# Kernel optimization log

Hardware: AMD Instinct MI355X
Metric: run time of the kernel (lower is better)

The kernel has to match this reference:

```python
import jax, jax.numpy as jnp
import numpy as np

E = 524288
B = 16
NODE_IN = 128
EDGE_IN = 64
GLOBAL_IN = 64
HIDDEN = 256
EDGE_OUT = 64
CAT_IN = EDGE_IN + 2 * NODE_IN + GLOBAL_IN  # 384


def setup_inputs() -> dict:
    key = jax.random.key(0)
    ks = jax.random.split(key, 9)
    src = jax.random.normal(ks[0], (E, NODE_IN), dtype=jnp.float32)
    dest = jax.random.normal(ks[1], (E, NODE_IN), dtype=jnp.float32)
    edge_attr = jax.random.normal(ks[2], (E, EDGE_IN), dtype=jnp.float32)
    u = jax.random.normal(ks[3], (B, GLOBAL_IN), dtype=jnp.float32)
    batch = jnp.sort(jax.random.randint(ks[4], (E,), 0, B, dtype=jnp.int64))
    # MLP params (torch Linear default init scale ~1/sqrt(fan_in))
    W1 = jax.random.normal(ks[5], (CAT_IN, HIDDEN), dtype=jnp.float32) / np.sqrt(CAT_IN)
    b1 = jax.random.normal(ks[6], (HIDDEN,), dtype=jnp.float32) / np.sqrt(CAT_IN)
    W2 = jax.random.normal(ks[7], (HIDDEN, EDGE_OUT), dtype=jnp.float32) / np.sqrt(HIDDEN)
    b2 = jax.random.normal(ks[8], (EDGE_OUT,), dtype=jnp.float32) / np.sqrt(HIDDEN)
    return {"src": src, "dest": dest, "edge_attr": edge_attr, "u": u,
            "batch": batch, "W1": W1, "b1": b1, "W2": W2, "b2": b2}


def reference(src, dest, edge_attr, u, batch, W1, b1, W2, b2):
    # gather global features per edge, concat, 2-layer MLP with ReLU
    x = jnp.concatenate([src, dest, edge_attr, u[batch]], axis=1)  # [E, 384]
    h = jax.nn.relu(x @ W1 + b1)                                   # [E, hidden]
    return h @ W2 + b2                                             # [E, edge_out]
```

## Files before the change

kernel.cpp:

```cpp
#include <hip/hip_runtime.h>

typedef __bf16 bf16_t;
typedef bf16_t bf16x8 __attribute__((ext_vector_type(8)));
typedef float f32x4 __attribute__((ext_vector_type(4)));
typedef unsigned short u16;
typedef u16 u16x8 __attribute__((ext_vector_type(8)));
typedef unsigned int u32;
typedef u32 u32x4 __attribute__((ext_vector_type(4)));

#define E_TOT 524288
#define MT 64
#define NBLK (E_TOT / MT)

__device__ __forceinline__ u16 f2bf(float f) {
  u32 u = __builtin_bit_cast(u32, f);
  u += 0x7FFFu + ((u >> 16) & 1u);
  return (u16)(u >> 16);
}

__device__ __forceinline__ u16x8 pack8(f32x4 a, f32x4 b) {
  u16x8 p;
  p[0] = f2bf(a[0]); p[1] = f2bf(a[1]); p[2] = f2bf(a[2]); p[3] = f2bf(a[3]);
  p[4] = f2bf(b[0]); p[5] = f2bf(b[1]); p[6] = f2bf(b[2]); p[7] = f2bf(b[3]);
  return p;
}

__global__ void prep_w1t(const float* __restrict__ W1, u16* __restrict__ W1T) {
  int t = blockIdx.x * 256 + threadIdx.x;
  if (t < 256 * 384) {
    int n = t / 384, k = t % 384;
    W1T[t] = f2bf(W1[k * 256 + n]);
  }
}
__global__ void prep_w2t(const float* __restrict__ W2, u16* __restrict__ W2T) {
  int t = blockIdx.x * 256 + threadIdx.x;
  if (t < 64 * 256) {
    int n = t / 256, k = t % 256;
    W2T[t] = f2bf(W2[k * 64 + n]);
  }
}

__global__ void __launch_bounds__(256) edge_fused(
    const float* __restrict__ src, const float* __restrict__ dst,
    const float* __restrict__ ea, const float* __restrict__ u,
    const int* __restrict__ batch, const u16* __restrict__ W1T,
    const float* __restrict__ b1, const u16* __restrict__ W2T,
    const float* __restrict__ b2, float* __restrict__ out)
{
  __shared__ __align__(16) u16 smem[32768];
  u16* As  = smem;
  u16* Ws  = smem + 4608;
  u16* Hs  = smem;
  u16* W2s = smem + 16384;

  const int t    = threadIdx.x;
  const int wid  = t >> 6;
  const int lane = t & 63;
  const int lr   = lane & 15;
  const int lg   = lane >> 4;
  const int e0   = blockIdx.x * MT;

  f32x4 acc[4][4];
  #pragma unroll
  for (int i = 0; i < 4; ++i)
    #pragma unroll
    for (int j = 0; j < 4; ++j)
      acc[i][j] = (f32x4){0.f, 0.f, 0.f, 0.f};

  const int r  = t >> 2;
  const int cg = (t & 3) << 4;

  #pragma unroll
  for (int kb = 0; kb < 6; ++kb) {
    __syncthreads();
    const float* rowp;
    if (kb < 2)       rowp = src + (e0 + r) * 128 + kb * 64;
    else if (kb < 4)  rowp = dst + (e0 + r) * 128 + (kb - 2) * 64;
    else if (kb == 4) rowp = ea + (e0 + r) * 64;
    else              rowp = u + batch[e0 + r] * 64;
    f32x4 v0 = *(const f32x4*)(rowp + cg + 0);
    f32x4 v1 = *(const f32x4*)(rowp + cg + 4);
    f32x4 v2 = *(const f32x4*)(rowp + cg + 8);
    f32x4 v3 = *(const f32x4*)(rowp + cg + 12);
    *(u16x8*)&As[r * 72 + cg + 0] = pack8(v0, v1);
    *(u16x8*)&As[r * 72 + cg + 8] = pack8(v2, v3);

    #pragma unroll
    for (int it = 0; it < 8; ++it) {
      int idx = t + it * 256;
      int n = idx >> 3, j = idx & 7;
      u32x4 d = *(const u32x4*)(W1T + n * 384 + kb * 64 + j * 8);
      *(u32x4*)&Ws[n * 72 + j * 8] = d;
    }
    __syncthreads();

    #pragma unroll
    for (int ks = 0; ks < 2; ++ks) {
      bf16x8 af[4], bfr[4];
      #pragma unroll
      for (int mf = 0; mf < 4; ++mf)
        af[mf] = *(const bf16x8*)&As[(mf * 16 + lr) * 72 + ks * 32 + lg * 8];
      #pragma unroll
      for (int nf = 0; nf < 4; ++nf)
        bfr[nf] = *(const bf16x8*)&Ws[(wid * 64 + nf * 16 + lr) * 72 + ks * 32 + lg * 8];
      #pragma unroll
      for (int mf = 0; mf < 4; ++mf)
        #pragma unroll
        for (int nf = 0; nf < 4; ++nf)
          acc[mf][nf] = __builtin_amdgcn_mfma_f32_16x16x32_bf16(af[mf], bfr[nf], acc[mf][nf], 0, 0, 0);
    }
  }
  __syncthreads();

  float bias[4];
  #pragma unroll
  for (int nf = 0; nf < 4; ++nf) bias[nf] = b1[wid * 64 + nf * 16 + lr];
  #pragma unroll
  for (int mf = 0; mf < 4; ++mf)
    #pragma unroll
    for (int nf = 0; nf < 4; ++nf)
      #pragma unroll
      for (int rr = 0; rr < 4; ++rr) {
        int row = mf * 16 + lg * 4 + rr;
        int col = wid * 64 + nf * 16 + lr;
        float v = fmaxf(acc[mf][nf][rr] + bias[nf], 0.f);
        Hs[row * 256 + ((((col >> 3) ^ (row & 7)) << 3) | (col & 7))] = f2bf(v);
      }

  #pragma unroll
  for (int it = 0; it < 8; ++it) {
    int idx = t + it * 256;
    int n = idx >> 5, j = idx & 31;
    u32x4 d = *(const u32x4*)(W2T + n * 256 + j * 8);
    *(u32x4*)&W2s[n * 256 + ((j ^ (n & 7)) << 3)] = d;
  }
  __syncthreads();

  f32x4 acc2[4];
  #pragma unroll
  for (int nf = 0; nf < 4; ++nf) acc2[nf] = (f32x4){0.f, 0.f, 0.f, 0.f};
  const int rowA = wid * 16 + lr;
  #pragma unroll
  for (int ks = 0; ks < 8; ++ks) {
    bf16x8 a = *(const bf16x8*)&Hs[rowA * 256 + (((ks * 4 + lg) ^ (rowA & 7)) << 3)];
    #pragma unroll
    for (int nf = 0; nf < 4; ++nf) {
      int n = nf * 16 + lr;
      bf16x8 b = *(const bf16x8*)&W2s[n * 256 + (((ks * 4 + lg) ^ (n & 7)) << 3)];
      acc2[nf] = __builtin_amdgcn_mfma_f32_16x16x32_bf16(a, b, acc2[nf], 0, 0, 0);
    }
  }

  #pragma unroll
  for (int nf = 0; nf < 4; ++nf) {
    float bb = b2[nf * 16 + lr];
    #pragma unroll
    for (int rr = 0; rr < 4; ++rr) {
      int row = e0 + wid * 16 + lg * 4 + rr;
      out[row * 64 + nf * 16 + lr] = acc2[nf][rr] + bb;
    }
  }
}

extern "C" void kernel_launch(void* const* d_in, const int* in_sizes, int n_in,
                              void* d_out, int out_size, void* d_ws, size_t ws_size,
                              hipStream_t stream) {
  const float* src  = (const float*)d_in[0];
  const float* dst  = (const float*)d_in[1];
  const float* ea   = (const float*)d_in[2];
  const float* u    = (const float*)d_in[3];
  const int* batch  = (const int*)d_in[4];
  const float* W1   = (const float*)d_in[5];
  const float* b1   = (const float*)d_in[6];
  const float* W2   = (const float*)d_in[7];
  const float* b2   = (const float*)d_in[8];
  float* out = (float*)d_out;

  u16* W1T = (u16*)d_ws;
  u16* W2T = W1T + 256 * 384;

  prep_w1t<<<(256 * 384 + 255) / 256, 256, 0, stream>>>(W1, W1T);
  prep_w2t<<<(64 * 256 + 255) / 256, 256, 0, stream>>>(W2, W2T);
  edge_fused<<<NBLK, 256, 0, stream>>>(src, dst, ea, u, batch, W1T, b1, W2T, b2, out);
}
```

Baseline: 269.5 us.

## Double tile to 128 edges with 512-thread blocks and register prefetch of next k-block

Doubles the edge tile per block to 128 rows with 8 waves arranged 2x4, so each W1 k-slice staged in shared memory is reused across twice as many edges. It also prefetches the next k-block's inputs and weights into registers before the MFMA phase, overlapping global loads with compute. The second GEMM runs in two halves that reuse the hidden buffer, which adds extra barriers. Register pressure grows under launch_bounds(512,4) and may cause spills or lower occupancy.

```diff
diff --git a/kernel.cpp b/kernel.cpp
--- a/kernel.cpp
+++ b/kernel.cpp
@@ -9,7 +9,7 @@
 typedef u32 u32x4 __attribute__((ext_vector_type(4)));
 
 #define E_TOT 524288
-#define MT 64
+#define MT 128
 #define NBLK (E_TOT / MT)
 
 __device__ __forceinline__ u16 f2bf(float f) {
@@ -40,7 +40,7 @@
   }
 }
 
-__global__ void __launch_bounds__(256) edge_fused(
+__global__ void __launch_bounds__(512, 4) edge_fused(
     const float* __restrict__ src, const float* __restrict__ dst,
     const float* __restrict__ ea, const float* __restrict__ u,
     const int* __restrict__ batch, const u16* __restrict__ W1T,
@@ -49,7 +49,7 @@
 {
   __shared__ __align__(16) u16 smem[32768];
   u16* As  = smem;
-  u16* Ws  = smem + 4608;
+  u16* Ws  = smem + 9216;
   u16* Hs  = smem;
   u16* W2s = smem + 16384;
 
@@ -58,6 +58,8 @@
   const int lane = t & 63;
   const int lr   = lane & 15;
   const int lg   = lane >> 4;
+  const int wr   = wid >> 2;
+  const int wc   = wid & 3;
   const int e0   = blockIdx.x * MT;
 
   f32x4 acc[4][4];
@@ -70,95 +72,116 @@
   const int r  = t >> 2;
   const int cg = (t & 3) << 4;
 
+  f32x4 pa[4];
+  u32x4 pw[4];
+
+  auto issue = [&](int kb) {
+    const float* rowp;
+    if (kb < 2)       rowp = src + (size_t)(e0 + r) * 128 + kb * 64;
+    else if (kb < 4)  rowp = dst + (size_t)(e0 + r) * 128 + (kb - 2) * 64;
+    else if (kb == 4) rowp = ea + (size_t)(e0 + r) * 64;
+    else              rowp = u + (size_t)batch[e0 + r] * 64;
+    pa[0] = *(const f32x4*)(rowp + cg + 0);
+    pa[1] = *(const f32x4*)(rowp + cg + 4);
+    pa[2] = *(const f32x4*)(rowp + cg + 8);
+    pa[3] = *(const f32x4*)(rowp + cg + 12);
+    #pragma unroll
+    for (int it = 0; it < 4; ++it) {
+      int idx = t + it * 512;
+      int n = idx >> 3, j = idx & 7;
+      pw[it] = *(const u32x4*)(W1T + n * 384 + kb * 64 + j * 8);
+    }
+  };
+
+  issue(0);
+
   #pragma unroll
   for (int kb = 0; kb < 6; ++kb) {
     __syncthreads();
-    const float* rowp;
-    if (kb < 2)       rowp = src + (e0 + r) * 128 + kb * 64;
-    else if (kb < 4)  rowp = dst + (e0 + r) * 128 + (kb - 2) * 64;
-    else if (kb == 4) rowp = ea + (e0 + r) * 64;
-    else              rowp = u + batch[e0 + r] * 64;
-    f32x4 v0 = *(const f32x4*)(rowp + cg + 0);
-    f32x4 v1 = *(const f32x4*)(rowp + cg + 4);
-    f32x4 v2 = *(const f32x4*)(rowp + cg + 8);
-    f32x4 v3 = *(const f32x4*)(rowp + cg + 12);
-    *(u16x8*)&As[r * 72 + cg + 0] = pack8(v0, v1);
-    *(u16x8*)&As[r * 72 + cg + 8] = pack8(v2, v3);
-
-    #pragma unroll
-    for (int it = 0; it < 8; ++it) {
-      int idx = t + it * 256;
+    *(u16x8*)&As[r * 72 + cg + 0] = pack8(pa[0], pa[1]);
+    *(u16x8*)&As[r * 72 + cg + 8] = pack8(pa[2], pa[3]);
+    #pragma unroll
+    for (int it = 0; it < 4; ++it) {
+      int idx = t + it * 512;
       int n = idx >> 3, j = idx & 7;
-      u32x4 d = *(const u32x4*)(W1T + n * 384 + kb * 64 + j * 8);
-      *(u32x4*)&Ws[n * 72 + j * 8] = d;
-    }
+      *(u32x4*)&Ws[n * 72 + j * 8] = pw[it];
+    }
+    if (kb < 5) issue(kb + 1);
     __syncthreads();
 
     #pragma unroll
     for (int ks = 0; ks < 2; ++ks) {
-      bf16x8 af[4], bfr[4];
+      bf16x8 af[4];
       #pragma unroll
       for (int mf = 0; mf < 4; ++mf)
-        af[mf] = *(const bf16x8*)&As[(mf * 16 + lr) * 72 + ks * 32 + lg * 8];
+        af[mf] = *(const bf16x8*)&As[(wr * 64 + mf * 16 + lr) * 72 + ks * 32 + lg * 8];
       #pragma unroll
-      for (int nf = 0; nf < 4; ++nf)
-        bfr[nf] = *(const bf16x8*)&Ws[(wid * 64 + nf * 16 + lr) * 72 + ks * 32 + lg * 8];
+      for (int nf = 0; nf < 4; ++nf) {
+        bf16x8 bfr = *(const bf16x8*)&Ws[(wc * 64 + nf * 16 + lr) * 72 + ks * 32 + lg * 8];
+        #pragma unroll
+        for (int mf = 0; mf < 4; ++mf)
+          acc[mf][nf] = __builtin_amdgcn_mfma_f32_16x16x32_bf16(af[mf], bfr, acc[mf][nf], 0, 0, 0);
+      }
+    }
+  }
+  __syncthreads();
+
+  #pragma unroll
+  for (int it = 0; it < 4; ++it) {
+    int idx = t + it * 512;
+    int n = idx >> 5, j = idx & 31;
+    u32x4 d = *(const u32x4*)(W2T + n * 256 + j * 8);
+    *(u32x4*)&W2s[n * 256 + ((j ^ (n & 7)) << 3)] = d;
+  }
+
+  float bias1[4];
+  #pragma unroll
+  for (int nf = 0; nf < 4; ++nf) bias1[nf] = b1[wc * 64 + nf * 16 + lr];
+
+  const int mf2 = wid >> 1;
+  const int nf2a = (wid & 1) * 2;
+  const int nf2b = nf2a + 1;
+  const float bb_a = b2[nf2a * 16 + lr];
+  const float bb_b = b2[nf2b * 16 + lr];
+
+  #pragma unroll
+  for (int half = 0; half < 2; ++half) {
+    if (wr == half) {
       #pragma unroll
       for (int mf = 0; mf < 4; ++mf)
         #pragma unroll
         for (int nf = 0; nf < 4; ++nf)
-          acc[mf][nf] = __builtin_amdgcn_mfma_f32_16x16x32_bf16(af[mf], bfr[nf], acc[mf][nf], 0, 0, 0);
-    }
-  }
-  __syncthreads();
-
-  float bias[4];
-  #pragma unroll
-  for (int nf = 0; nf < 4; ++nf) bias[nf] = b1[wid * 64 + nf * 16 + lr];
-  #pragma unroll
-  for (int mf = 0; mf < 4; ++mf)
-    #pragma unroll
-    for (int nf = 0; nf < 4; ++nf)
-      #pragma unroll
-      for (int rr = 0; rr < 4; ++rr) {
-        int row = mf * 16 + lg * 4 + rr;
-        int col = wid * 64 + nf * 16 + lr;
-        float v = fmaxf(acc[mf][nf][rr] + bias[nf], 0.f);
-        Hs[row * 256 + ((((col >> 3) ^ (row & 7)) << 3) | (col & 7))] = f2bf(v);
-      }
-
-  #pragma unroll
-  for (int it = 0; it < 8; ++it) {
-    int idx = t + it * 256;
-    int n = idx >> 5, j = idx & 31;
-    u32x4 d = *(const u32x4*)(W2T + n * 256 + j * 8);
-    *(u32x4*)&W2s[n * 256 + ((j ^ (n & 7)) << 3)] = d;
-  }
-  __syncthreads();
-
-  f32x4 acc2[4];
-  #pragma unroll
-  for (int nf = 0; nf < 4; ++nf) acc2[nf] = (f32x4){0.f, 0.f, 0.f, 0.f};
-  const int rowA = wid * 16 + lr;
-  #pragma unroll
-  for (int ks = 0; ks < 8; ++ks) {
-    bf16x8 a = *(const bf16x8*)&Hs[rowA * 256 + (((ks * 4 + lg) ^ (rowA & 7)) << 3)];
-    #pragma unroll
-    for (int nf = 0; nf < 4; ++nf) {
-      int n = nf * 16 + lr;
-      bf16x8 b = *(const bf16x8*)&W2s[n * 256 + (((ks * 4 + lg) ^ (n & 7)) << 3)];
-      acc2[nf] = __builtin_amdgcn_mfma_f32_16x16x32_bf16(a, b, acc2[nf], 0, 0, 0);
-    }
-  }
-
-  #pragma unroll
-  for (int nf = 0; nf < 4; ++nf) {
-    float bb = b2[nf * 16 + lr];
+          #pragma unroll
+          for (int rr = 0; rr < 4; ++rr) {
+            int row = mf * 16 + lg * 4 + rr;
+            int col = wc * 64 + nf * 16 + lr;
+            float v = fmaxf(acc[mf][nf][rr] + bias1[nf], 0.f);
+            Hs[row * 256 + ((((col >> 3) ^ (row & 7)) << 3) | (col & 7))] = f2bf(v);
+          }
+    }
+    __syncthreads();
+
+    f32x4 acc2a = (f32x4){0.f, 0.f, 0.f, 0.f};
+    f32x4 acc2b = (f32x4){0.f, 0.f, 0.f, 0.f};
+    const int rowA = mf2 * 16 + lr;
+    #pragma unroll
+    for (int ks = 0; ks < 8; ++ks) {
+      bf16x8 a = *(const bf16x8*)&Hs[rowA * 256 + (((ks * 4 + lg) ^ (rowA & 7)) << 3)];
+      int nA = nf2a * 16 + lr;
+      int nB = nf2b * 16 + lr;
+      bf16x8 ba = *(const bf16x8*)&W2s[nA * 256 + (((ks * 4 + lg) ^ (nA & 7)) << 3)];
+      bf16x8 bb = *(const bf16x8*)&W2s[nB * 256 + (((ks * 4 + lg) ^ (nB & 7)) << 3)];
+      acc2a = __builtin_amdgcn_mfma_f32_16x16x32_bf16(a, ba, acc2a, 0, 0, 0);
+      acc2b = __builtin_amdgcn_mfma_f32_16x16x32_bf16(a, bb, acc2b, 0, 0, 0);
+    }
+
     #pragma unroll
     for (int rr = 0; rr < 4; ++rr) {
-      int row = e0 + wid * 16 + lg * 4 + rr;
-      out[row * 64 + nf * 16 + lr] = acc2[nf][rr] + bb;
-    }
+      int row = e0 + half * 64 + mf2 * 16 + lg * 4 + rr;
+      out[row * 64 + nf2a * 16 + lr] = acc2a[rr] + bb_a;
+      out[row * 64 + nf2b * 16 + lr] = acc2b[rr] + bb_b;
+    }
+    __syncthreads();
   }
 }
 
@@ -181,5 +204,5 @@
 
   prep_w1t<<<(256 * 384 + 255) / 256, 256, 0, stream>>>(W1, W1T);
   prep_w2t<<<(64 * 256 + 255) / 256, 256, 0, stream>>>(W2, W2T);
-  edge_fused<<<NBLK, 256, 0, stream>>>(src, dst, ea, u, batch, W1T, b1, W2T, b2, out);
-}
+  edge_fused<<<NBLK, 512, 0, stream>>>(src, dst, ea, u, batch, W1T, b1, W2T, b2, out);
+}
```

Result: slower. 524.6 us (+94.7%).

## Prefetch A tiles into registers, direct-to-LDS W1 loads, swizzled layout, W2 from global

Applied to the files above, without the earlier changes.

Pre-swizzles W1 on the host-side prep kernel so each K-block tile can be copied straight into LDS with global_load_lds. Replaces the padded stride-72 LDS layouts with XOR-swizzled stride-64 layouts. Issues the next A-tile's global loads before the current MFMA step so memory latency overlaps compute. Drops the W2 LDS staging in favour of reading W2 directly from global/cache in the second GEMM. Together these shrink LDS use, which may allow more resident blocks, but the direct W2 global reads may add latency and the explicit vmcnt(0) wait also waits on the prefetched A loads.

```diff
diff --git a/kernel.cpp b/kernel.cpp
--- a/kernel.cpp
+++ b/kernel.cpp
@@ -25,13 +25,23 @@
   return p;
 }
 
-__global__ void prep_w1t(const float* __restrict__ W1, u16* __restrict__ W1T) {
+__device__ __forceinline__ void gload_lds16(const void* g, void* l) {
+  __builtin_amdgcn_global_load_lds(
+      (const __attribute__((address_space(1))) u32*)g,
+      (__attribute__((address_space(3))) u32*)l, 16, 0, 0);
+}
+
+__global__ void prep_w1ts(const float* __restrict__ W1, u16* __restrict__ W1Ts) {
   int t = blockIdx.x * 256 + threadIdx.x;
-  if (t < 256 * 384) {
-    int n = t / 384, k = t % 384;
-    W1T[t] = f2bf(W1[k * 256 + n]);
-  }
-}
+  if (t < 384 * 256) {
+    int U = t >> 3, e = t & 7;
+    int kb = U >> 11, rem = U & 2047;
+    int n = rem >> 3, jswz = rem & 7;
+    int k = kb * 64 + ((jswz ^ (n & 7)) << 3) + e;
+    W1Ts[t] = f2bf(W1[k * 256 + n]);
+  }
+}
+
 __global__ void prep_w2t(const float* __restrict__ W2, u16* __restrict__ W2T) {
   int t = blockIdx.x * 256 + threadIdx.x;
   if (t < 64 * 256) {
@@ -43,15 +53,14 @@
 __global__ void __launch_bounds__(256) edge_fused(
     const float* __restrict__ src, const float* __restrict__ dst,
     const float* __restrict__ ea, const float* __restrict__ u,
-    const int* __restrict__ batch, const u16* __restrict__ W1T,
+    const int* __restrict__ batch, const u16* __restrict__ W1Ts,
     const float* __restrict__ b1, const u16* __restrict__ W2T,
     const float* __restrict__ b2, float* __restrict__ out)
 {
-  __shared__ __align__(16) u16 smem[32768];
-  u16* As  = smem;
-  u16* Ws  = smem + 4608;
-  u16* Hs  = smem;
-  u16* W2s = smem + 16384;
+  __shared__ __align__(16) u16 smem[20480];
+  u16* As = smem;
+  u16* Ws = smem + 4096;
+  u16* Hs = smem;
 
   const int t    = threadIdx.x;
   const int wid  = t >> 6;
@@ -70,51 +79,67 @@
   const int r  = t >> 2;
   const int cg = (t & 3) << 4;
 
+  f32x4 pa[4];
+  auto issueA = [&](int kb) {
+    const float* rowp;
+    if (kb < 2)       rowp = src + (size_t)(e0 + r) * 128 + kb * 64;
+    else if (kb < 4)  rowp = dst + (size_t)(e0 + r) * 128 + (kb - 2) * 64;
+    else if (kb == 4) rowp = ea + (size_t)(e0 + r) * 64;
+    else              rowp = u + (size_t)batch[e0 + r] * 64;
+    pa[0] = *(const f32x4*)(rowp + cg + 0);
+    pa[1] = *(const f32x4*)(rowp + cg + 4);
+    pa[2] = *(const f32x4*)(rowp + cg + 8);
+    pa[3] = *(const f32x4*)(rowp + cg + 12);
+  };
+
+  issueA(0);
+
   #pragma unroll
   for (int kb = 0; kb < 6; ++kb) {
     __syncthreads();
-    const float* rowp;
-    if (kb < 2)       rowp = src + (e0 + r) * 128 + kb * 64;
-    else if (kb < 4)  rowp = dst + (e0 + r) * 128 + (kb - 2) * 64;
-    else if (kb == 4) rowp = ea + (e0 + r) * 64;
-    else              rowp = u + batch[e0 + r] * 64;
-    f32x4 v0 = *(const f32x4*)(rowp + cg + 0);
-    f32x4 v1 = *(const f32x4*)(rowp + cg + 4);
-    f32x4 v2 = *(const f32x4*)(rowp + cg + 8);
-    f32x4 v3 = *(const f32x4*)(rowp + cg + 12);
-    *(u16x8*)&As[r * 72 + cg + 0] = pack8(v0, v1);
-    *(u16x8*)&As[r * 72 + cg + 8] = pack8(v2, v3);
+
+    {
+      u16x8 lo = pack8(pa[0], pa[1]);
+      u16x8 hi = pack8(pa[2], pa[3]);
+      int j0 = (t & 3) * 2;
+      *(u16x8*)&As[r * 64 + ((j0 ^ (r & 7)) << 3)]       = lo;
+      *(u16x8*)&As[r * 64 + (((j0 + 1) ^ (r & 7)) << 3)] = hi;
+    }
 
     #pragma unroll
     for (int it = 0; it < 8; ++it) {
-      int idx = t + it * 256;
-      int n = idx >> 3, j = idx & 7;
-      u32x4 d = *(const u32x4*)(W1T + n * 384 + kb * 64 + j * 8);
-      *(u32x4*)&Ws[n * 72 + j * 8] = d;
-    }
+      int ubase = (it * 4 + wid) * 64;
+      gload_lds16(W1Ts + ((size_t)kb * 2048 + ubase + lane) * 8,
+                  &Ws[ubase * 8]);
+    }
+    asm volatile("s_waitcnt vmcnt(0)" ::: "memory");
     __syncthreads();
 
+    if (kb < 5) issueA(kb + 1);
+
     #pragma unroll
     for (int ks = 0; ks < 2; ++ks) {
-      bf16x8 af[4], bfr[4];
+      bf16x8 af[4];
       #pragma unroll
-      for (int mf = 0; mf < 4; ++mf)
-        af[mf] = *(const bf16x8*)&As[(mf * 16 + lr) * 72 + ks * 32 + lg * 8];
+      for (int mf = 0; mf < 4; ++mf) {
+        int row = mf * 16 + lr;
+        af[mf] = *(const bf16x8*)&As[row * 64 + (((ks * 4 + lg) ^ (row & 7)) << 3)];
+      }
       #pragma unroll
-      for (int nf = 0; nf < 4; ++nf)
-        bfr[nf] = *(const bf16x8*)&Ws[(wid * 64 + nf * 16 + lr) * 72 + ks * 32 + lg * 8];
-      #pragma unroll
-      for (int mf = 0; mf < 4; ++mf)
+      for (int nf = 0; nf < 4; ++nf) {
+        int n = wid * 64 + nf * 16 + lr;
+        bf16x8 bfr = *(const bf16x8*)&Ws[n * 64 + (((ks * 4 + lg) ^ (n & 7)) << 3)];
         #pragma unroll
-        for (int nf = 0; nf < 4; ++nf)
-          acc[mf][nf] = __builtin_amdgcn_mfma_f32_16x16x32_bf16(af[mf], bfr[nf], acc[mf][nf], 0, 0, 0);
+        for (int mf = 0; mf < 4; ++mf)
+          acc[mf][nf] = __builtin_amdgcn_mfma_f32_16x16x32_bf16(af[mf], bfr, acc[mf][nf], 0, 0, 0);
+      }
     }
   }
   __syncthreads();
 
-  float bias[4];
-  #pragma unroll
-  for (int nf = 0; nf < 4; ++nf) bias[nf] = b1[wid * 64 + nf * 16 + lr];
+  float bias1[4];
+  #pragma unroll
+  for (int nf = 0; nf < 4; ++nf) bias1[nf] = b1[wid * 64 + nf * 16 + lr];
   #pragma unroll
   for (int mf = 0; mf < 4; ++mf)
     #pragma unroll
@@ -123,17 +148,9 @@
       for (int rr = 0; rr < 4; ++rr) {
         int row = mf * 16 + lg * 4 + rr;
         int col = wid * 64 + nf * 16 + lr;
-        float v = fmaxf(acc[mf][nf][rr] + bias[nf], 0.f);
+        float v = fmaxf(acc[mf][nf][rr] + bias1[nf], 0.f);
         Hs[row * 256 + ((((col >> 3) ^ (row & 7)) << 3) | (col & 7))] = f2bf(v);
       }
-
-  #pragma unroll
-  for (int it = 0; it < 8; ++it) {
-    int idx = t + it * 256;
-    int n = idx >> 5, j = idx & 31;
-    u32x4 d = *(const u32x4*)(W2T + n * 256 + j * 8);
-    *(u32x4*)&W2s[n * 256 + ((j ^ (n & 7)) << 3)] = d;
-  }
   __syncthreads();
 
   f32x4 acc2[4];
@@ -146,7 +163,7 @@
     #pragma unroll
     for (int nf = 0; nf < 4; ++nf) {
       int n = nf * 16 + lr;
-      bf16x8 b = *(const bf16x8*)&W2s[n * 256 + (((ks * 4 + lg) ^ (n & 7)) << 3)];
+      bf16x8 b = *(const bf16x8*)(W2T + n * 256 + ks * 32 + lg * 8);
       acc2[nf] = __builtin_amdgcn_mfma_f32_16x16x32_bf16(a, b, acc2[nf], 0, 0, 0);
     }
   }
@@ -157,7 +174,7 @@
     #pragma unroll
     for (int rr = 0; rr < 4; ++rr) {
       int row = e0 + wid * 16 + lg * 4 + rr;
-      out[row * 64 + nf * 16 + lr] = acc2[nf][rr] + bb;
+      out[(size_t)row * 64 + nf * 16 + lr] = acc2[nf][rr] + bb;
     }
   }
 }
@@ -176,10 +193,10 @@
   const float* b2   = (const float*)d_in[8];
   float* out = (float*)d_out;
 
-  u16* W1T = (u16*)d_ws;
-  u16* W2T = W1T + 256 * 384;
-
-  prep_w1t<<<(256 * 384 + 255) / 256, 256, 0, stream>>>(W1, W1T);
+  u16* W1Ts = (u16*)d_ws;
+  u16* W2T  = W1Ts + 384 * 256;
+
+  prep_w1ts<<<(384 * 256 + 255) / 256, 256, 0, stream>>>(W1, W1Ts);
   prep_w2t<<<(64 * 256 + 255) / 256, 256, 0, stream>>>(W2, W2T);
-  edge_fused<<<NBLK, 256, 0, stream>>>(src, dst, ea, u, batch, W1T, b1, W2T, b2, out);
-}
+  edge_fused<<<NBLK, 256, 0, stream>>>(src, dst, ea, u, batch, W1Ts, b1, W2T, b2, out);
+}
```

New measurement: 313.8 us. 1.16x slower.
